# Kernel tuning notes

Hardware: AMD Instinct MI355X
Metric: run time of the kernel (lower is better)

## Reference

```python
import math
import jax, jax.numpy as jnp
import numpy as np

B, C, NX, NY = 8, 16, 512, 512
N = 16384
N_RES, NH, S = 90, 5, 0.5


def _normal(x, mu, s):
    # exp(-0.5*((x-mu)/s)^2) / (sqrt(s^2) * sqrt(2*pi))  -- matches torch helper
    return jnp.exp(-0.5 * ((x - mu) / s) ** 2) / (jnp.sqrt(s * s) * math.sqrt(2.0 * math.pi))


def setup_inputs() -> dict:
    key = jax.random.key(0)
    k1, k2 = jax.random.split(key)
    x = jax.random.normal(k1, (B, C, NX, NY), dtype=jnp.float32)
    coords = jax.random.uniform(k2, (B, N, 2), dtype=jnp.float32)
    nh_m = (NH - 1) / 2 + 0.5
    pixel_offset_normal = jnp.linspace(nh_m, -nh_m, N_RES, dtype=jnp.float32)
    pixel_offset_indices = jnp.linspace(-(NH - 1) // 2, (NH - 1) // 2, NH, dtype=jnp.float32)
    s = jnp.float32(S)
    return {"x": x, "coords": coords, "s": s,
            "pixel_offset_normal": pixel_offset_normal,
            "pixel_offset_indices": pixel_offset_indices}


def reference(x, coords, s, pixel_offset_normal, pixel_offset_indices):
    b, n, _ = coords.shape
    _, c, nx, ny = x.shape
    nh = pixel_offset_indices.shape[0]

    # continuous positions in pixel space
    px = coords[:, :, 1] * (nx - 1)   # [b,n]
    py = coords[:, :, 0] * (ny - 1)
    rpx, rpy = jnp.round(px), jnp.round(py)

    # gaussian weights integrated over sub-pixel resolution (n_res samples -> nh bins)
    # NOTE: torch code clamps both axes with x.shape[-2] (=nx); replicated faithfully.
    pxo = jnp.clip(rpx[..., None] - pixel_offset_normal, 0.0, nx)   # [b,n,n_res]
    pyo = jnp.clip(rpy[..., None] - pixel_offset_normal, 0.0, nx)
    wx = _normal(pxo, px[..., None], s).reshape(b, n, nh, -1).sum(-1)  # [b,n,nh]
    wy = _normal(pyo, py[..., None], s).reshape(b, n, nh, -1).sum(-1)
    w2d = wx[..., :, None] * wy[..., None, :]                          # [b,n,nh,nh]
    w2d = w2d / w2d.reshape(b, n, -1).sum(-1)[..., None, None]

    # integer neighborhood indices (both axes clamped with nx-1, as in torch code)
    ix = jnp.clip(jnp.round(rpx[..., None] - pixel_offset_indices), 0, nx - 1).astype(jnp.int32)  # [b,n,nh]
    iy = jnp.clip(jnp.round(rpy[..., None] - pixel_offset_indices), 0, nx - 1).astype(jnp.int32)

    # per-batch gather of nh x nh neighborhoods (equivalent to torch's BxB gather + diagonal)
    flat = (ix[..., :, None] * ny + iy[..., None, :]).reshape(b, n * nh * nh)  # [b, n*nh*nh]
    xf = x.reshape(b, c, nx * ny)
    g = jax.vmap(lambda xi, idx: xi[:, idx])(xf, flat)       # [b,c,n*nh*nh]
    g = g.reshape(b, c, n, nh, nh)

    out = (g * w2d[:, None]).reshape(b, c, n, nh * nh).sum(-1)  # [b,c,n]
    return out
```

## Files before the change

### kernel.cpp

```cpp
#include <hip/hip_runtime.h>

#define BV    8
#define CV    16
#define NXV   512
#define NYV   512
#define NV    16384
#define NRES  90
#define NHV   5
#define TPB   256

#define NPTS  (BV * NV)
#define TSH   6
#define TDIM  (NXV >> TSH)
#define NBUCKB (TDIM * TDIM)
#define NBUCK  (BV * NBUCKB)

#define RROWS 68
#define RSEG  18
#define ROWB  (RSEG * 16)
#define SLOTS (RROWS * RSEG)

#if __has_builtin(__builtin_amdgcn_exp2f)
#define EXP2 __builtin_amdgcn_exp2f
#else
#define EXP2 exp2f
#endif

__global__ void zero_counts_kernel(int* __restrict__ counts) {
    counts[threadIdx.x] = 0;
}

__device__ __forceinline__ int bucket_key(float rpx, float rpy, int i) {
    const int tr = ((int)rpx) >> TSH;
    const int tc = ((int)rpy) >> TSH;
    return (i >> 14) * NBUCKB + tr * TDIM + tc;
}

__global__ __launch_bounds__(TPB) void bucket_count_kernel(
    const float* __restrict__ coords, int* __restrict__ counts)
{
    const int i = blockIdx.x * TPB + threadIdx.x;
    const float2 cd = *(const float2*)(coords + (size_t)i * 2);
    const float rpx = rintf(cd.y * (float)(NXV - 1));
    const float rpy = rintf(cd.x * (float)(NYV - 1));
    atomicAdd(&counts[bucket_key(rpx, rpy, i)], 1);
}

__global__ __launch_bounds__(NBUCK) void scan_kernel(
    const int* __restrict__ counts, int* __restrict__ starts,
    int* __restrict__ cursors)
{
    __shared__ int sm[NBUCK];
    const int tid = threadIdx.x;
    const int v = counts[tid];
    sm[tid] = v;
    __syncthreads();
    #pragma unroll
    for (int off = 1; off < NBUCK; off <<= 1) {
        int t = sm[tid];
        if (tid >= off) t += sm[tid - off];
        __syncthreads();
        sm[tid] = t;
        __syncthreads();
    }
    const int e = sm[tid] - v;
    starts[tid]  = e;
    cursors[tid] = e;
}

__global__ __launch_bounds__(TPB) void scatter_weights_kernel(
    const float* __restrict__ coords,
    const float* __restrict__ s_ptr,
    const float* __restrict__ offn,
    const float* __restrict__ offi,
    int* __restrict__ cursors,
    float4* __restrict__ w8a, float4* __restrict__ w8b,
    float4* __restrict__ wx4, int4* __restrict__ off4,
    float4* __restrict__ misc)
{
    const int i = blockIdx.x * TPB + threadIdx.x;

    const float2 cd = *(const float2*)(coords + (size_t)i * 2);
    const float px  = cd.y * (float)(NXV - 1);
    const float py  = cd.x * (float)(NYV - 1);
    const float rpx = rintf(px);
    const float rpy = rintf(py);

    const int pos = atomicAdd(&cursors[bucket_key(rpx, rpy, i)], 1);

    const float s = s_ptr[0];
    const float k = -0.72134752044448169f / (s * s);

    float wx[NHV], wy[NHV];
    float sx = 0.f, sy = 0.f;
    #pragma unroll
    for (int h = 0; h < NHV; ++h) {
        float ax = 0.f, ay = 0.f;
        #pragma unroll 6
        for (int t = 0; t < NRES / NHV; ++t) {
            const float off = offn[h * (NRES / NHV) + t];
            const float vx = fminf(fmaxf(rpx - off, 0.f), (float)NXV);
            const float vy = fminf(fmaxf(rpy - off, 0.f), (float)NXV);
            const float dx = vx - px;
            const float dy = vy - py;
            ax += EXP2(k * dx * dx);
            ay += EXP2(k * dy * dy);
        }
        wx[h] = ax; wy[h] = ay;
        sx += ax;  sy += ay;
    }
    const float inv = 1.0f / (sx * sy);

    int ix[NHV], iy[NHV];
    #pragma unroll
    for (int h = 0; h < NHV; ++h) {
        const float fo = offi[h];
        ix[h] = (int)fminf(fmaxf(rintf(rpx - fo), 0.f), (float)(NXV - 1));
        iy[h] = (int)fminf(fmaxf(rintf(rpy - fo), 0.f), (float)(NXV - 1));
    }

    const int a = min(iy[NHV - 1] & ~3, NYV - 8);

    float w8[8];
    #pragma unroll
    for (int kk = 0; kk < 8; ++kk) {
        float w = 0.f;
        #pragma unroll
        for (int j = 0; j < NHV; ++j)
            w += (iy[j] - a == kk) ? wy[j] * inv : 0.f;
        w8[kk] = w;
    }

    w8a[pos] = make_float4(w8[0], w8[1], w8[2], w8[3]);
    w8b[pos] = make_float4(w8[4], w8[5], w8[6], w8[7]);
    wx4[pos] = make_float4(wx[0], wx[1], wx[2], wx[3]);
    off4[pos] = make_int4((ix[0] * NYV + a) * 4, (ix[1] * NYV + a) * 4,
                          (ix[2] * NYV + a) * 4, (ix[3] * NYV + a) * 4);
    misc[pos] = make_float4(wx[4], __int_as_float((ix[4] * NYV + a) * 4),
                            __int_as_float(i), 0.f);
}

__global__ __launch_bounds__(TPB, 8) void tile_gather_kernel(
    const float* __restrict__ x,
    const int* __restrict__ starts, const int* __restrict__ ends,
    const float4* __restrict__ w8a, const float4* __restrict__ w8b,
    const float4* __restrict__ wx4, const int4* __restrict__ off4,
    const float4* __restrict__ misc,
    float* __restrict__ out)
{
    __shared__ float4 lds[SLOTS];

    const int bid = blockIdx.x;
    const int c   = blockIdx.y;
    const int b   = bid >> 6;
    const int tr  = (bid >> 3) & (TDIM - 1);
    const int tc  = bid & (TDIM - 1);
    const int r0  = tr << TSH, c0 = tc << TSH;
    const int R0  = min(max(r0 - 2, 0), NXV - RROWS);
    const int W0  = min(max(c0 - 4, 0), NYV - RSEG * 4);

    const int tid = threadIdx.x;
    const char* bx = (const char*)x + ((size_t)(b * CV + c) << 20);

    #pragma unroll
    for (int kk = 0; kk < (SLOTS + TPB - 1) / TPB; ++kk) {
        const int slot = tid + kk * TPB;
        if (slot < SLOTS) {
            const int row = slot / RSEG;
            const int seg = slot - row * RSEG;
            lds[slot] = *(const float4*)(bx + ((size_t)(R0 + row) << 11)
                                            + (W0 << 2) + (seg << 4));
        }
    }
    __syncthreads();

    const int s0 = starts[bid];
    const int e1 = ends[bid];
    const char* ldsb = (const char*)lds;
    const int base0 = -R0 * ROWB - (W0 << 2);

    for (int p = s0 + tid; p < e1; p += TPB) {
        const float4 wa = w8a[p];
        const float4 wb = w8b[p];
        const float4 wr = wx4[p];
        const int4   o4 = off4[p];
        const float4 ms = misc[p];
        const float  we = ms.x;
        const int    oe = __float_as_int(ms.y);
        const int    i  = __float_as_int(ms.z);
        const int    n  = i & (NV - 1);

        float acc = 0.f;
#define ROW(OFF, WROW) {                                                     \
        const int lo = base0 + ((OFF) >> 11) * ROWB + ((OFF) & 2047);        \
        const float4 va = *(const float4*)(ldsb + lo);                       \
        const float4 vb = *(const float4*)(ldsb + lo + 16);                  \
        const float rs = va.x * wa.x + va.y * wa.y + va.z * wa.z +           \
                         va.w * wa.w + vb.x * wb.x + vb.y * wb.y +           \
                         vb.z * wb.z + vb.w * wb.w;                          \
        acc = fmaf(WROW, rs, acc); }

        ROW(o4.x, wr.x)
        ROW(o4.y, wr.y)
        ROW(o4.z, wr.z)
        ROW(o4.w, wr.w)
        ROW(oe,   we)
#undef ROW

        out[(((size_t)(b * CV + c)) << 14) + n] = acc;
    }
}

extern "C" void kernel_launch(void* const* d_in, const int* in_sizes, int n_in,
                              void* d_out, int out_size, void* d_ws, size_t ws_size,
                              hipStream_t stream) {
    const float* x      = (const float*)d_in[0];
    const float* coords = (const float*)d_in[1];
    const float* s_ptr  = (const float*)d_in[2];
    const float* offn   = (const float*)d_in[3];
    const float* offi   = (const float*)d_in[4];
    float* out = (float*)d_out;

    char* w = (char*)d_ws;
    float4* w8a  = (float4*)w;  w += (size_t)NPTS * 16;
    float4* w8b  = (float4*)w;  w += (size_t)NPTS * 16;
    float4* wx4  = (float4*)w;  w += (size_t)NPTS * 16;
    int4*   off4 = (int4*)w;    w += (size_t)NPTS * 16;
    float4* misc = (float4*)w;  w += (size_t)NPTS * 16;
    int*    counts  = (int*)w;  w += (size_t)NBUCK * 4;
    int*    starts  = (int*)w;  w += (size_t)NBUCK * 4;
    int*    cursors = (int*)w;

    zero_counts_kernel<<<dim3(1), dim3(NBUCK), 0, stream>>>(counts);
    bucket_count_kernel<<<dim3(NPTS / TPB), dim3(TPB), 0, stream>>>(coords, counts);
    scan_kernel<<<dim3(1), dim3(NBUCK), 0, stream>>>(counts, starts, cursors);
    scatter_weights_kernel<<<dim3(NPTS / TPB), dim3(TPB), 0, stream>>>(
        coords, s_ptr, offn, offi, cursors, w8a, w8b, wx4, off4, misc);

    dim3 grid(NBUCK, CV, 1);
    tile_gather_kernel<<<grid, dim3(TPB), 0, stream>>>(
        x, starts, cursors, w8a, w8b, wx4, off4, misc, out);
}
```

Measured before the change: 300.9 us.

## Process four tile-channel pairs per workgroup with register-prefetched LDS staging

After: 387.7 us. 1.29x slower.

```diff
diff --git a/kernel.cpp b/kernel.cpp
--- a/kernel.cpp
+++ b/kernel.cpp
@@ -19,6 +19,11 @@
 #define RSEG  18
 #define ROWB  (RSEG * 16)
 #define SLOTS (RROWS * RSEG)
+#define SROUNDS ((SLOTS + TPB - 1) / TPB)
+
+#define NPAIR (NBUCK * CV)
+#define PAIRS 4
+#define NWG   (NPAIR / PAIRS)
 
 #if __has_builtin(__builtin_amdgcn_exp2f)
 #define EXP2 __builtin_amdgcn_exp2f
@@ -140,6 +145,28 @@
                             __int_as_float(i), 0.f);
 }
 
+__device__ __forceinline__ void load_pair_regs(
+    const float* __restrict__ x, int pr, int tid, float4 (&r)[SROUNDS])
+{
+    const int tile = pr >> 4, ch = pr & (CV - 1);
+    const int b  = tile >> 6;
+    const int tr = (tile >> 3) & (TDIM - 1);
+    const int tc = tile & (TDIM - 1);
+    const int R0 = min(max((tr << TSH) - 2, 0), NXV - RROWS);
+    const int W0 = min(max((tc << TSH) - 4, 0), NYV - RSEG * 4);
+    const char* bx = (const char*)x + ((size_t)(b * CV + ch) << 20);
+    #pragma unroll
+    for (int k = 0; k < SROUNDS; ++k) {
+        const int slot = tid + k * TPB;
+        if (slot < SLOTS) {
+            const int row = slot / RSEG;
+            const int seg = slot - row * RSEG;
+            r[k] = *(const float4*)(bx + ((size_t)(R0 + row) << 11)
+                                       + (W0 << 2) + (seg << 4));
+        }
+    }
+}
+
 __global__ __launch_bounds__(TPB, 8) void tile_gather_kernel(
     const float* __restrict__ x,
     const int* __restrict__ starts, const int* __restrict__ ends,
@@ -149,48 +176,51 @@
     float* __restrict__ out)
 {
     __shared__ float4 lds[SLOTS];
-
-    const int bid = blockIdx.x;
-    const int c   = blockIdx.y;
-    const int b   = bid >> 6;
-    const int tr  = (bid >> 3) & (TDIM - 1);
-    const int tc  = bid & (TDIM - 1);
-    const int r0  = tr << TSH, c0 = tc << TSH;
-    const int R0  = min(max(r0 - 2, 0), NXV - RROWS);
-    const int W0  = min(max(c0 - 4, 0), NYV - RSEG * 4);
-
     const int tid = threadIdx.x;
-    const char* bx = (const char*)x + ((size_t)(b * CV + c) << 20);
-
-    #pragma unroll
-    for (int kk = 0; kk < (SLOTS + TPB - 1) / TPB; ++kk) {
-        const int slot = tid + kk * TPB;
-        if (slot < SLOTS) {
-            const int row = slot / RSEG;
-            const int seg = slot - row * RSEG;
-            lds[slot] = *(const float4*)(bx + ((size_t)(R0 + row) << 11)
-                                            + (W0 << 2) + (seg << 4));
-        }
-    }
-    __syncthreads();
-
-    const int s0 = starts[bid];
-    const int e1 = ends[bid];
-    const char* ldsb = (const char*)lds;
-    const int base0 = -R0 * ROWB - (W0 << 2);
-
-    for (int p = s0 + tid; p < e1; p += TPB) {
-        const float4 wa = w8a[p];
-        const float4 wb = w8b[p];
-        const float4 wr = wx4[p];
-        const int4   o4 = off4[p];
-        const float4 ms = misc[p];
-        const float  we = ms.x;
-        const int    oe = __float_as_int(ms.y);
-        const int    i  = __float_as_int(ms.z);
-        const int    n  = i & (NV - 1);
-
-        float acc = 0.f;
+
+    const int g = (blockIdx.x & 7) * (NWG / 8) + (blockIdx.x >> 3);
+    const int pair0 = g * PAIRS;
+
+    float4 r[SROUNDS];
+    load_pair_regs(x, pair0, tid, r);
+
+    #pragma unroll
+    for (int t = 0; t < PAIRS; ++t) {
+        const int pr   = pair0 + t;
+        const int tile = pr >> 4;
+        const int ch   = pr & (CV - 1);
+        const int b    = tile >> 6;
+        const int tr   = (tile >> 3) & (TDIM - 1);
+        const int tc   = tile & (TDIM - 1);
+        const int R0   = min(max((tr << TSH) - 2, 0), NXV - RROWS);
+        const int W0   = min(max((tc << TSH) - 4, 0), NYV - RSEG * 4);
+
+        #pragma unroll
+        for (int k = 0; k < SROUNDS; ++k) {
+            const int slot = tid + k * TPB;
+            if (slot < SLOTS) lds[slot] = r[k];
+        }
+        if (t + 1 < PAIRS) load_pair_regs(x, pr + 1, tid, r);
+
+        __syncthreads();
+
+        const int s0 = starts[tile];
+        const int e1 = ends[tile];
+        const char* ldsb = (const char*)lds;
+        const int base0 = -R0 * ROWB - (W0 << 2);
+
+        for (int p = s0 + tid; p < e1; p += TPB) {
+            const float4 wa = w8a[p];
+            const float4 wb = w8b[p];
+            const float4 wr = wx4[p];
+            const int4   o4 = off4[p];
+            const float4 ms = misc[p];
+            const float  we = ms.x;
+            const int    oe = __float_as_int(ms.y);
+            const int    i  = __float_as_int(ms.z);
+            const int    n  = i & (NV - 1);
+
+            float acc = 0.f;
 #define ROW(OFF, WROW) {                                                     \
         const int lo = base0 + ((OFF) >> 11) * ROWB + ((OFF) & 2047);        \
         const float4 va = *(const float4*)(ldsb + lo);                       \
@@ -200,14 +230,16 @@
                          vb.z * wb.z + vb.w * wb.w;                          \
         acc = fmaf(WROW, rs, acc); }
 
-        ROW(o4.x, wr.x)
-        ROW(o4.y, wr.y)
-        ROW(o4.z, wr.z)
-        ROW(o4.w, wr.w)
-        ROW(oe,   we)
+            ROW(o4.x, wr.x)
+            ROW(o4.y, wr.y)
+            ROW(o4.z, wr.z)
+            ROW(o4.w, wr.w)
+            ROW(oe,   we)
 #undef ROW
 
-        out[(((size_t)(b * CV + c)) << 14) + n] = acc;
+            out[(((size_t)(b * CV + ch)) << 14) + n] = acc;
+        }
+        __syncthreads();
     }
 }
 
@@ -237,7 +269,6 @@
     scatter_weights_kernel<<<dim3(NPTS / TPB), dim3(TPB), 0, stream>>>(
         coords, s_ptr, offn, offi, cursors, w8a, w8b, wx4, off4, misc);
 
-    dim3 grid(NBUCK, CV, 1);
-    tile_gather_kernel<<<grid, dim3(TPB), 0, stream>>>(
+    tile_gather_kernel<<<dim3(NWG), dim3(TPB), 0, stream>>>(
         x, starts, cursors, w8a, w8b, wx4, off4, misc, out);
 }
```
